# Optimization experiments

Measured on AMD Instinct MI355X. Metric: run time of the kernel, lower is better.

## Reference

```python
import jax, jax.numpy as jnp
import numpy as np

B, D_IN, H, D_OUT = 8192, 1024, 4096, 1024


def setup_inputs() -> dict:
    key = jax.random.key(0)
    ks = jax.random.split(key, 8)
    return {
        "X": jax.random.normal(ks[0], (B, D_IN), jnp.float32),
        "state": jax.random.normal(ks[1], (B, H), jnp.float32),
        "W_in": jax.random.normal(ks[2], (H, D_IN), jnp.float32) * (2.0 / D_IN) ** 0.5,
        "b_in": jax.random.normal(ks[3], (H,), jnp.float32) * 0.1,
        "W_rec": jax.random.normal(ks[4], (H, H), jnp.float32) * (2.0 / H) ** 0.5,
        "b_rec": jax.random.normal(ks[5], (H,), jnp.float32) * 0.1,
        "W_out": jax.random.normal(ks[6], (D_OUT, H), jnp.float32) * (2.0 / H) ** 0.5,
        "b_out": jax.random.normal(ks[7], (D_OUT,), jnp.float32) * 0.1,
    }


def reference(X, state, W_in, b_in, W_rec, b_rec, W_out, b_out):
    # Single vanilla RNN cell step (ReLU recurrence), matching VanillaRNN.forward.
    # state: [B, H] = ReLU(X @ W_in^T + b_in + state @ W_rec^T + b_rec)
    new_state = jax.nn.relu(X @ W_in.T + b_in + state @ W_rec.T + b_rec)
    # out: [B, D_OUT] = ReLU(new_state @ W_out^T + b_out)
    out = jax.nn.relu(new_state @ W_out.T + b_out)
    return out, new_state
```

## Files before the change

kernel.cpp:

```cpp
#include <hip/hip_runtime.h>
#include <hip/hip_bf16.h>
#include <stdint.h>
#include <stddef.h>

#define BSZ  8192
#define DIN  1024
#define HH   4096
#define DOUT 1024

#define BM 128
#define BN 128
#define BK 32

typedef __attribute__((ext_vector_type(8))) short   frag8;
typedef __attribute__((ext_vector_type(4))) float   f32x4;
typedef __attribute__((ext_vector_type(8))) unsigned short u16x8;

__device__ __forceinline__ unsigned short f2bf_rne(float f) {
    union { float f; uint32_t u; } c; c.f = f;
    uint32_t u = c.u;
    return (unsigned short)((u + 0x7FFFu + ((u >> 16) & 1u)) >> 16);
}

__device__ __forceinline__ void cvt8(const float* __restrict__ s, unsigned short* __restrict__ d) {
    f32x4 v0 = *(const f32x4*)s;
    f32x4 v1 = *(const f32x4*)(s + 4);
    u16x8 o;
    o[0] = f2bf_rne(v0[0]); o[1] = f2bf_rne(v0[1]); o[2] = f2bf_rne(v0[2]); o[3] = f2bf_rne(v0[3]);
    o[4] = f2bf_rne(v1[0]); o[5] = f2bf_rne(v1[1]); o[6] = f2bf_rne(v1[2]); o[7] = f2bf_rne(v1[3]);
    *(u16x8*)d = o;
}

__global__ __launch_bounds__(256)
void cvt_f32_bf16(const float* __restrict__ src, unsigned short* __restrict__ dst, long n) {
    long i = ((long)blockIdx.x * 256 + threadIdx.x) * 8;
    if (i < n) cvt8(src + i, dst + i);
}

__global__ __launch_bounds__(256)
void cvt_all5(const float* __restrict__ s0, unsigned short* __restrict__ d0, long n0,
              const float* __restrict__ s1, unsigned short* __restrict__ d1, long n1,
              const float* __restrict__ s2, unsigned short* __restrict__ d2, long n2,
              const float* __restrict__ s3, unsigned short* __restrict__ d3, long n3,
              const float* __restrict__ s4, unsigned short* __restrict__ d4, long n4) {
    long i = ((long)blockIdx.x * 256 + threadIdx.x) * 8;
    if (i < n0) { cvt8(s0 + i, d0 + i); return; } i -= n0;
    if (i < n1) { cvt8(s1 + i, d1 + i); return; } i -= n1;
    if (i < n2) { cvt8(s2 + i, d2 + i); return; } i -= n2;
    if (i < n3) { cvt8(s3 + i, d3 + i); return; } i -= n3;
    if (i < n4) { cvt8(s4 + i, d4 + i); }
}

__device__ __forceinline__ void glds16(const unsigned short* __restrict__ gp, short* lp) {
    __builtin_amdgcn_global_load_lds(
        (const __attribute__((address_space(1))) uint32_t*)gp,
        (__attribute__((address_space(3))) uint32_t*)lp, 16, 0, 0);
}

template <bool A_BF16, bool B_BF16>
__global__ __launch_bounds__(256)
void gemm_bt_relu(const void* __restrict__ A1, int lda1,
                  const void* __restrict__ A2, int lda2,
                  const void* __restrict__ B1, int ldb1,
                  const void* __restrict__ B2, int ldb2,
                  int Ksplit, int K,
                  const float* __restrict__ bias1, const float* __restrict__ bias2,
                  float* __restrict__ C, unsigned short* __restrict__ Cb, int N) {
    __shared__ short As[BM * BK];
    __shared__ short Bs[BN * BK];

    const int tid    = threadIdx.x;
    const int tile_m = blockIdx.y * BM;
    const int tile_n = blockIdx.x * BN;
    const int wave = tid >> 6, lane = tid & 63;
    const int quad = lane >> 4, l16 = lane & 15;
    const int wm = (wave >> 1) * 64;
    const int wn = (wave & 1) * 64;
    const int sr = tid >> 2;
    const int sc = (tid & 3) * 8;

    short* ldsA0 = &As[tid * 8]; short* ldsA1 = &As[(256 + tid) * 8];
    short* ldsB0 = &Bs[tid * 8]; short* ldsB1 = &Bs[(256 + tid) * 8];

    f32x4 acc[4][4] = {};

    for (int phase = 0; phase < 2; ++phase) {
        const int kmax = phase ? (K - Ksplit) : Ksplit;
        if (kmax <= 0) continue;
        const void* Ap = phase ? A2 : A1; const int la = phase ? lda2 : lda1;
        const void* Bp = phase ? B2 : B1; const int lb = phase ? ldb2 : ldb1;

        const unsigned short *ga = nullptr, *gb = nullptr;
        const float *fa = nullptr, *fb = nullptr;
        if (A_BF16) ga = (const unsigned short*)Ap + (size_t)(tile_m + sr) * la + sc;
        else        fa = (const float*)Ap          + (size_t)(tile_m + sr) * la + sc;
        if (B_BF16) gb = (const unsigned short*)Bp + (size_t)(tile_n + sr) * lb + sc;
        else        fb = (const float*)Bp          + (size_t)(tile_n + sr) * lb + sc;
        const size_t la64 = (size_t)64 * la, lb64 = (size_t)64 * lb;

        for (int kk = 0; kk < kmax; kk += BK) {
            __syncthreads();
            if (A_BF16) {
                glds16(ga, ldsA0); glds16(ga + la64, ldsA1); ga += BK;
            } else {
                unsigned short t0[8], t1[8];
                cvt8(fa, t0); cvt8(fa + la64, t1); fa += BK;
                *(u16x8*)ldsA0 = *(u16x8*)t0; *(u16x8*)ldsA1 = *(u16x8*)t1;
            }
            if (B_BF16) {
                glds16(gb, ldsB0); glds16(gb + lb64, ldsB1); gb += BK;
            } else {
                unsigned short t0[8], t1[8];
                cvt8(fb, t0); cvt8(fb + lb64, t1); fb += BK;
                *(u16x8*)ldsB0 = *(u16x8*)t0; *(u16x8*)ldsB1 = *(u16x8*)t1;
            }
            __syncthreads();

            frag8 af[4], bfr[4];
#pragma unroll
            for (int i = 0; i < 4; i++)
                af[i] = *(const frag8*)&As[(wm + i * 16 + l16) * BK + quad * 8];
#pragma unroll
            for (int i = 0; i < 4; i++)
                bfr[i] = *(const frag8*)&Bs[(wn + i * 16 + l16) * BK + quad * 8];
#pragma unroll
            for (int mi = 0; mi < 4; mi++)
#pragma unroll
                for (int ni = 0; ni < 4; ni++)
                    acc[mi][ni] = __builtin_amdgcn_mfma_f32_16x16x32_bf16(
                        af[mi], bfr[ni], acc[mi][ni], 0, 0, 0);
        }
    }

#pragma unroll
    for (int mi = 0; mi < 4; mi++) {
        const int m0 = tile_m + wm + mi * 16 + quad * 4;
#pragma unroll
        for (int ni = 0; ni < 4; ni++) {
            const int n = tile_n + wn + ni * 16 + l16;
            float bv = bias1[n];
            if (bias2) bv += bias2[n];
#pragma unroll
            for (int r = 0; r < 4; r++) {
                float v = acc[mi][ni][r] + bv;
                v = v > 0.f ? v : 0.f;
                const size_t idx = (size_t)(m0 + r) * N + n;
                C[idx] = v;
                if (Cb) Cb[idx] = f2bf_rne(v);
            }
        }
    }
}

extern "C" void kernel_launch(void* const* d_in, const int* in_sizes, int n_in,
                              void* d_out, int out_size, void* d_ws, size_t ws_size,
                              hipStream_t stream) {
    const float* X     = (const float*)d_in[0];
    const float* state = (const float*)d_in[1];
    const float* W_in  = (const float*)d_in[2];
    const float* b_in  = (const float*)d_in[3];
    const float* W_rec = (const float*)d_in[4];
    const float* b_rec = (const float*)d_in[5];
    const float* W_out = (const float*)d_in[6];
    const float* b_out = (const float*)d_in[7];

    float* out       = (float*)d_out;
    float* new_state = out + (size_t)BSZ * DOUT;

    const size_t nX = (size_t)BSZ * DIN, nS = (size_t)BSZ * HH;
    const size_t nWin = (size_t)HH * DIN, nWrec = (size_t)HH * HH, nWout = (size_t)DOUT * HH;

    const size_t offX = 0;
    const size_t offS = offX + nX * 2;
    const size_t offWin = offS + nS * 2;
    const size_t offWrec = offWin + nWin * 2;
    const size_t offWout = offWrec + nWrec * 2;
    const size_t offNS = offWout + nWout * 2;
    const size_t need_full = offNS + nS * 2;
    const size_t need_mid = nS * 2 + nWout * 2;

    char* ws = (char*)d_ws;
    const dim3 blk(256);
    const dim3 g1(HH / BN, BSZ / BM);
    const dim3 g2(DOUT / BN, BSZ / BM);

    if (ws_size >= need_full) {
        unsigned short* Xb    = (unsigned short*)(ws + offX);
        unsigned short* Sb    = (unsigned short*)(ws + offS);
        unsigned short* Winb  = (unsigned short*)(ws + offWin);
        unsigned short* Wrecb = (unsigned short*)(ws + offWrec);
        unsigned short* Woutb = (unsigned short*)(ws + offWout);
        unsigned short* NSb   = (unsigned short*)(ws + offNS);
        const long total = (long)(nX + nS + nWin + nWrec + nWout);
        cvt_all5<<<dim3((unsigned)((total / 8 + 255) / 256)), blk, 0, stream>>>(
            X, Xb, (long)nX, state, Sb, (long)nS, W_in, Winb, (long)nWin,
            W_rec, Wrecb, (long)nWrec, W_out, Woutb, (long)nWout);
        gemm_bt_relu<true, true><<<g1, blk, 0, stream>>>(
            Xb, DIN, Sb, HH, Winb, DIN, Wrecb, HH, DIN, DIN + HH,
            b_in, b_rec, new_state, NSb, HH);
        gemm_bt_relu<true, true><<<g2, blk, 0, stream>>>(
            NSb, HH, NSb, HH, Woutb, HH, Woutb, HH, HH, HH,
            b_out, nullptr, out, nullptr, DOUT);
    } else if (ws_size >= need_mid) {
        unsigned short* NSb   = (unsigned short*)ws;
        unsigned short* Woutb = (unsigned short*)(ws + nS * 2);
        cvt_f32_bf16<<<dim3((unsigned)((nWout / 8 + 255) / 256)), blk, 0, stream>>>(
            W_out, Woutb, (long)nWout);
        gemm_bt_relu<false, false><<<g1, blk, 0, stream>>>(
            X, DIN, state, HH, W_in, DIN, W_rec, HH, DIN, DIN + HH,
            b_in, b_rec, new_state, NSb, HH);
        gemm_bt_relu<true, true><<<g2, blk, 0, stream>>>(
            NSb, HH, NSb, HH, Woutb, HH, Woutb, HH, HH, HH,
            b_out, nullptr, out, nullptr, DOUT);
    } else {
        gemm_bt_relu<false, false><<<g1, blk, 0, stream>>>(
            X, DIN, state, HH, W_in, DIN, W_rec, HH, DIN, DIN + HH,
            b_in, b_rec, new_state, nullptr, HH);
        gemm_bt_relu<false, false><<<g2, blk, 0, stream>>>(
            new_state, HH, new_state, HH, W_out, HH, W_out, HH, HH, HH,
            b_out, nullptr, out, nullptr, DOUT);
    }
}
```

Baseline: 897.2 us.

## Split-K the output GEMM into two halves with a separate bias-ReLU reduction

The output projection GEMM now runs with a z-dimension of two, each block covering half of the hidden dimension and writing raw fp32 partial sums into the workspace, which reuses the bf16 input staging area. A new elementwise kernel sums the two partials, adds the output bias and applies ReLU. This doubles the number of blocks for the smaller GEMM to fill the GPU better. In exchange it adds a partial-sum buffer write/read and an extra kernel launch.

Result: slower. 926.4 us (+3.3%).

```diff
diff --git a/kernel.cpp b/kernel.cpp
--- a/kernel.cpp
+++ b/kernel.cpp
@@ -51,19 +51,43 @@
     if (i < n4) { cvt8(s4 + i, d4 + i); }
 }
 
+__global__ __launch_bounds__(256)
+void reduce2_bias_relu(const float* __restrict__ P, const float* __restrict__ bias,
+                       float* __restrict__ out, long total, int N) {
+    long i = ((long)blockIdx.x * 256 + threadIdx.x) * 8;
+    if (i >= total) return;
+    f32x4 a0 = *(const f32x4*)(P + i);
+    f32x4 a1 = *(const f32x4*)(P + i + 4);
+    f32x4 b0 = *(const f32x4*)(P + total + i);
+    f32x4 b1 = *(const f32x4*)(P + total + i + 4);
+    const int n = (int)(i & (long)(N - 1));
+    f32x4 c0 = *(const f32x4*)(bias + n);
+    f32x4 c1 = *(const f32x4*)(bias + n + 4);
+    f32x4 r0, r1;
+#pragma unroll
+    for (int j = 0; j < 4; j++) {
+        float v0 = a0[j] + b0[j] + c0[j];
+        float v1 = a1[j] + b1[j] + c1[j];
+        r0[j] = v0 > 0.f ? v0 : 0.f;
+        r1[j] = v1 > 0.f ? v1 : 0.f;
+    }
+    *(f32x4*)(out + i) = r0;
+    *(f32x4*)(out + i + 4) = r1;
+}
+
 __device__ __forceinline__ void glds16(const unsigned short* __restrict__ gp, short* lp) {
     __builtin_amdgcn_global_load_lds(
         (const __attribute__((address_space(1))) uint32_t*)gp,
         (__attribute__((address_space(3))) uint32_t*)lp, 16, 0, 0);
 }
 
-template <bool A_BF16, bool B_BF16>
+template <bool A_BF16, bool B_BF16, bool FINAL>
 __global__ __launch_bounds__(256)
 void gemm_bt_relu(const void* __restrict__ A1, int lda1,
                   const void* __restrict__ A2, int lda2,
                   const void* __restrict__ B1, int ldb1,
                   const void* __restrict__ B2, int ldb2,
-                  int Ksplit, int K,
+                  int Ksplit, int K, int Kper,
                   const float* __restrict__ bias1, const float* __restrict__ bias2,
                   float* __restrict__ C, unsigned short* __restrict__ Cb, int N) {
     __shared__ short As[BM * BK];
@@ -72,6 +96,7 @@
     const int tid    = threadIdx.x;
     const int tile_m = blockIdx.y * BM;
     const int tile_n = blockIdx.x * BN;
+    const int kb     = blockIdx.z * Kper;
     const int wave = tid >> 6, lane = tid & 63;
     const int quad = lane >> 4, l16 = lane & 15;
     const int wm = (wave >> 1) * 64;
@@ -85,17 +110,21 @@
     f32x4 acc[4][4] = {};
 
     for (int phase = 0; phase < 2; ++phase) {
-        const int kmax = phase ? (K - Ksplit) : Ksplit;
+        const int ps = phase ? (kb > Ksplit ? kb : Ksplit) : kb;
+        const int pe_raw = kb + Kper;
+        const int pe = phase ? pe_raw : (pe_raw < Ksplit ? pe_raw : Ksplit);
+        const int kmax = pe - ps;
         if (kmax <= 0) continue;
+        const int kloc = phase ? (ps - Ksplit) : ps;
         const void* Ap = phase ? A2 : A1; const int la = phase ? lda2 : lda1;
         const void* Bp = phase ? B2 : B1; const int lb = phase ? ldb2 : ldb1;
 
         const unsigned short *ga = nullptr, *gb = nullptr;
         const float *fa = nullptr, *fb = nullptr;
-        if (A_BF16) ga = (const unsigned short*)Ap + (size_t)(tile_m + sr) * la + sc;
-        else        fa = (const float*)Ap          + (size_t)(tile_m + sr) * la + sc;
-        if (B_BF16) gb = (const unsigned short*)Bp + (size_t)(tile_n + sr) * lb + sc;
-        else        fb = (const float*)Bp          + (size_t)(tile_n + sr) * lb + sc;
+        if (A_BF16) ga = (const unsigned short*)Ap + (size_t)(tile_m + sr) * la + kloc + sc;
+        else        fa = (const float*)Ap          + (size_t)(tile_m + sr) * la + kloc + sc;
+        if (B_BF16) gb = (const unsigned short*)Bp + (size_t)(tile_n + sr) * lb + kloc + sc;
+        else        fb = (const float*)Bp          + (size_t)(tile_n + sr) * lb + kloc + sc;
         const size_t la64 = (size_t)64 * la, lb64 = (size_t)64 * lb;
 
         for (int kk = 0; kk < kmax; kk += BK) {
@@ -132,21 +161,26 @@
         }
     }
 
+    float* Cdst = C;
+    if (!FINAL) Cdst = C + (size_t)blockIdx.z * ((size_t)gridDim.y * BM) * N;
 #pragma unroll
     for (int mi = 0; mi < 4; mi++) {
         const int m0 = tile_m + wm + mi * 16 + quad * 4;
 #pragma unroll
         for (int ni = 0; ni < 4; ni++) {
             const int n = tile_n + wn + ni * 16 + l16;
-            float bv = bias1[n];
-            if (bias2) bv += bias2[n];
+            float bv = 0.f;
+            if (FINAL) {
+                bv = bias1[n];
+                if (bias2) bv += bias2[n];
+            }
 #pragma unroll
             for (int r = 0; r < 4; r++) {
                 float v = acc[mi][ni][r] + bv;
-                v = v > 0.f ? v : 0.f;
+                if (FINAL) v = v > 0.f ? v : 0.f;
                 const size_t idx = (size_t)(m0 + r) * N + n;
-                C[idx] = v;
-                if (Cb) Cb[idx] = f2bf_rne(v);
+                Cdst[idx] = v;
+                if (FINAL && Cb) Cb[idx] = f2bf_rne(v);
             }
         }
     }
@@ -182,6 +216,7 @@
     char* ws = (char*)d_ws;
     const dim3 blk(256);
     const dim3 g1(HH / BN, BSZ / BM);
+    const dim3 g2s(DOUT / BN, BSZ / BM, 2);
     const dim3 g2(DOUT / BN, BSZ / BM);
 
     if (ws_size >= need_full) {
@@ -191,33 +226,37 @@
         unsigned short* Wrecb = (unsigned short*)(ws + offWrec);
         unsigned short* Woutb = (unsigned short*)(ws + offWout);
         unsigned short* NSb   = (unsigned short*)(ws + offNS);
+        float*          Part  = (float*)(ws + offX);
         const long total = (long)(nX + nS + nWin + nWrec + nWout);
         cvt_all5<<<dim3((unsigned)((total / 8 + 255) / 256)), blk, 0, stream>>>(
             X, Xb, (long)nX, state, Sb, (long)nS, W_in, Winb, (long)nWin,
             W_rec, Wrecb, (long)nWrec, W_out, Woutb, (long)nWout);
-        gemm_bt_relu<true, true><<<g1, blk, 0, stream>>>(
-            Xb, DIN, Sb, HH, Winb, DIN, Wrecb, HH, DIN, DIN + HH,
+        gemm_bt_relu<true, true, true><<<g1, blk, 0, stream>>>(
+            Xb, DIN, Sb, HH, Winb, DIN, Wrecb, HH, DIN, DIN + HH, DIN + HH,
             b_in, b_rec, new_state, NSb, HH);
-        gemm_bt_relu<true, true><<<g2, blk, 0, stream>>>(
-            NSb, HH, NSb, HH, Woutb, HH, Woutb, HH, HH, HH,
-            b_out, nullptr, out, nullptr, DOUT);
+        gemm_bt_relu<true, true, false><<<g2s, blk, 0, stream>>>(
+            NSb, HH, NSb, HH, Woutb, HH, Woutb, HH, HH, HH, HH / 2,
+            nullptr, nullptr, Part, nullptr, DOUT);
+        const long totOut = (long)BSZ * DOUT;
+        reduce2_bias_relu<<<dim3((unsigned)((totOut / 8 + 255) / 256)), blk, 0, stream>>>(
+            Part, b_out, out, totOut, DOUT);
     } else if (ws_size >= need_mid) {
         unsigned short* NSb   = (unsigned short*)ws;
         unsigned short* Woutb = (unsigned short*)(ws + nS * 2);
         cvt_f32_bf16<<<dim3((unsigned)((nWout / 8 + 255) / 256)), blk, 0, stream>>>(
             W_out, Woutb, (long)nWout);
-        gemm_bt_relu<false, false><<<g1, blk, 0, stream>>>(
-            X, DIN, state, HH, W_in, DIN, W_rec, HH, DIN, DIN + HH,
+        gemm_bt_relu<false, false, true><<<g1, blk, 0, stream>>>(
+            X, DIN, state, HH, W_in, DIN, W_rec, HH, DIN, DIN + HH, DIN + HH,
             b_in, b_rec, new_state, NSb, HH);
-        gemm_bt_relu<true, true><<<g2, blk, 0, stream>>>(
-            NSb, HH, NSb, HH, Woutb, HH, Woutb, HH, HH, HH,
+        gemm_bt_relu<true, true, true><<<g2, blk, 0, stream>>>(
+            NSb, HH, NSb, HH, Woutb, HH, Woutb, HH, HH, HH, HH,
             b_out, nullptr, out, nullptr, DOUT);
     } else {
-        gemm_bt_relu<false, false><<<g1, blk, 0, stream>>>(
-            X, DIN, state, HH, W_in, DIN, W_rec, HH, DIN, DIN + HH,
+        gemm_bt_relu<false, false, true><<<g1, blk, 0, stream>>>(
+            X, DIN, state, HH, W_in, DIN, W_rec, HH, DIN, DIN + HH, DIN + HH,
             b_in, b_rec, new_state, nullptr, HH);
-        gemm_bt_relu<false, false><<<g2, blk, 0, stream>>>(
-            new_state, HH, new_state, HH, W_out, HH, W_out, HH, HH, HH,
+        gemm_bt_relu<false, false, true><<<g2, blk, 0, stream>>>(
+            new_state, HH, new_state, HH, W_out, HH, W_out, HH, HH, HH, HH,
             b_out, nullptr, out, nullptr, DOUT);
     }
 }
```
